# Performance work log

Hardware: AMD Instinct MI355X
Metric: run time of the kernel (lower is better)

Reference implementation:

```python
import jax, jax.numpy as jnp
import numpy as np

USER_NUM = 100000
ITEM_NUM = 50000
N_NODES = USER_NUM + ITEM_NUM
EMB = 64
NNZ = 5_000_000


def setup_inputs() -> dict:
    key = jax.random.key(0)
    k1, k2, k3, k4, k5 = jax.random.split(key, 5)
    user_emb = jax.random.normal(k1, (USER_NUM, EMB), dtype=jnp.float32) * 0.1
    item_emb = jax.random.normal(k2, (ITEM_NUM, EMB), dtype=jnp.float32) * 0.1
    adj_row = jax.random.randint(k3, (NNZ,), 0, N_NODES, dtype=jnp.int32)
    adj_col = jax.random.randint(k4, (NNZ,), 0, N_NODES, dtype=jnp.int32)
    # normalized-adjacency-like positive values
    adj_vals = jax.random.uniform(k5, (NNZ,), dtype=jnp.float32) / 32.0
    return {
        "user_emb": user_emb,
        "item_emb": item_emb,
        "adj_row": adj_row,
        "adj_col": adj_col,
        "adj_vals": adj_vals,
        "n_layers": 3,
    }


def _spmm(row, col, vals, x, n):
    # y = A @ x with A in COO: gather source rows, scale, scatter-add to dest rows
    gathered = x[col] * vals[:, None]  # [nnz, emb]
    return jax.ops.segment_sum(gathered, row, num_segments=n)


def reference(user_emb, item_emb, adj_row, adj_col, adj_vals, n_layers):
    ego = jnp.concatenate([user_emb, item_emb], axis=0)  # [N, emb]
    acc = ego  # running sum over layer outputs (fused stack+mean)
    for _ in range(n_layers):
        ego = _spmm(adj_row, adj_col, adj_vals, ego, N_NODES)
        acc = acc + ego
    all_emb = acc / jnp.asarray(n_layers + 1, dtype=acc.dtype)
    return all_emb[:USER_NUM], all_emb[USER_NUM:]
```

## Files before the change

### kernel.cpp

```cpp
#include <hip/hip_runtime.h>

#define USER_NUM 100000
#define ITEM_NUM 50000
#define N_NODES  150000
#define EMB      64
#define NNZ      5000000
#define NELEM    (N_NODES * EMB)

#define K        1024
#define RPB      147
#define T        8192
#define BST      512
#define NT       ((NNZ + T - 1) / T)
#define SB_CAP   8192

typedef float     vf4 __attribute__((ext_vector_type(4)));
typedef _Float16  vh4 __attribute__((ext_vector_type(4)));
typedef _Float16  half_t;

__global__ void concat_kernel(const float* __restrict__ user,
                              const float* __restrict__ item,
                              float* __restrict__ A, half_t* __restrict__ H0) {
    int i = blockIdx.x * blockDim.x + threadIdx.x;
    if (i >= NELEM / 4) return;
    int base = i * 4;
    const float* src = (base < USER_NUM * EMB) ? (user + base)
                                               : (item + (base - USER_NUM * EMB));
    vf4 v = __builtin_nontemporal_load((const vf4*)src);
    __builtin_nontemporal_store(v, (vf4*)(A + base));
    vh4 h;
    h[0] = (half_t)v[0]; h[1] = (half_t)v[1]; h[2] = (half_t)v[2]; h[3] = (half_t)v[3];
    __builtin_nontemporal_store(h, (vh4*)(H0 + base));
}

__global__ __launch_bounds__(256) void hist_kernel(const int* __restrict__ row,
                                                   int* __restrict__ bucketcnt) {
    __shared__ int h[K];
    for (int i = threadIdx.x; i < K; i += 256) h[i] = 0;
    __syncthreads();
    int stride = gridDim.x * 256;
    for (int e = blockIdx.x * 256 + threadIdx.x; e < NNZ; e += stride) {
        int b = __builtin_nontemporal_load(row + e) / RPB;
        atomicAdd(&h[b], 1);
    }
    __syncthreads();
    for (int i = threadIdx.x; i < K; i += 256)
        if (h[i]) atomicAdd(&bucketcnt[i], h[i]);
}

__global__ __launch_bounds__(256) void scan_buckets(const int* __restrict__ bucketcnt,
                                                    int* __restrict__ gbase,
                                                    int* __restrict__ gcursor) {
    __shared__ int c4[K];
    __shared__ int ps[256];
    int t = threadIdx.x;
    for (int i = t; i < K; i += 256) c4[i] = bucketcnt[i];
    __syncthreads();
    int s = c4[4*t] + c4[4*t+1] + c4[4*t+2] + c4[4*t+3];
    ps[t] = s;
    __syncthreads();
    for (int ofs = 1; ofs < 256; ofs <<= 1) {
        int tv = (t >= ofs) ? ps[t - ofs] : 0;
        __syncthreads();
        ps[t] += tv;
        __syncthreads();
    }
    int run = ps[t] - s;
    for (int k = 0; k < 4; ++k) {
        int b = 4*t + k;
        gbase[b] = run; gcursor[b] = run;
        run += c4[b];
    }
    if (t == 255) gbase[K] = run;
}

__global__ __launch_bounds__(BST) void bin_scatter(const int* __restrict__ row,
                                                   const int* __restrict__ col,
                                                   const float* __restrict__ vals,
                                                   int* __restrict__ gcursor,
                                                   long long* __restrict__ sedge) {
    __shared__ long long      staged[T];
    __shared__ int            srow[T];
    __shared__ unsigned short bs[T];
    __shared__ int cnt[K];
    __shared__ int cbase[K];
    __shared__ int gb[K];
    __shared__ int ps[BST];
    int tid = threadIdx.x;
    int e0 = blockIdx.x * T;
    int e1 = e0 + T; if (e1 > NNZ) e1 = NNZ;
    int n = e1 - e0;

    for (int i = tid; i < K; i += BST) cnt[i] = 0;
    __syncthreads();
    for (int e = e0 + tid; e < e1; e += BST) {
        int r = __builtin_nontemporal_load(row + e);
        srow[e - e0] = r;
        atomicAdd(&cnt[r / RPB], 1);
    }
    __syncthreads();
    int b0 = 2 * tid, b1 = b0 + 1;
    int c0 = cnt[b0], c1 = cnt[b1];
    int s = c0 + c1;
    ps[tid] = s;
    __syncthreads();
    for (int ofs = 1; ofs < BST; ofs <<= 1) {
        int tv = (tid >= ofs) ? ps[tid - ofs] : 0;
        __syncthreads();
        ps[tid] += tv;
        __syncthreads();
    }
    int run = ps[tid] - s;
    cbase[b0] = run;       cbase[b1] = run + c0;
    gb[b0] = c0 ? atomicAdd(&gcursor[b0], c0) : 0;
    gb[b1] = c1 ? atomicAdd(&gcursor[b1], c1) : 0;
    cnt[b0] = run;         cnt[b1] = run + c0;
    __syncthreads();
    for (int i = tid; i < n; i += BST) {
        int   r = srow[i];
        int   c = __builtin_nontemporal_load(col + e0 + i);
        float v = __builtin_nontemporal_load(vals + e0 + i);
        int b  = r / RPB;
        int ro = r - b * RPB;
        int slot = atomicAdd(&cnt[b], 1);
        staged[slot] = (long long)(unsigned)(c | (ro << 18))
                     | ((long long)__float_as_int(v) << 32);
        bs[slot] = (unsigned short)b;
    }
    __syncthreads();
    for (int i = tid; i < n; i += BST) {
        int b = bs[i];
        long long pv = staged[i];
        int dst = gb[b] + (i - cbase[b]);
        __builtin_nontemporal_store(pv, sedge + dst);
    }
}

__global__ __launch_bounds__(256) void sort_bucket(const int* __restrict__ gbase,
                                                   long long* __restrict__ sedge,
                                                   int* __restrict__ rowend,
                                                   long long* __restrict__ gscratch) {
    __shared__ long long staged[SB_CAP];
    __shared__ int rcnt[RPB];
    __shared__ int rbase[RPB + 1];
    __shared__ int rcur[RPB];
    int b = blockIdx.x;
    int s = gbase[b], e = gbase[b + 1];
    int n = e - s;
    int rowbase = b * RPB;
    int nr = N_NODES - rowbase;
    if (nr > RPB) nr = RPB;
    if (nr < 0) nr = 0;
    int tid = threadIdx.x;
    for (int i = tid; i < RPB; i += 256) rcnt[i] = 0;
    __syncthreads();
    for (int i = tid; i < n; i += 256) {
        int ro = (int)((sedge[s + i] >> 18) & 0xFF);
        atomicAdd(&rcnt[ro], 1);
    }
    __syncthreads();
    if (tid == 0) {
        int run = 0;
        for (int i = 0; i < RPB; ++i) { rbase[i] = run; run += rcnt[i]; }
        rbase[RPB] = run;
    }
    __syncthreads();
    for (int i = tid; i < nr; i += 256)
        rowend[rowbase + i] = s + rbase[i + 1];
    for (int i = tid; i < RPB; i += 256) rcur[i] = rbase[i];
    __syncthreads();
    if (n <= SB_CAP) {
        for (int i = tid; i < n; i += 256) {
            long long p = sedge[s + i];
            int ro = (int)((p >> 18) & 0xFF);
            int slot = atomicAdd(&rcur[ro], 1);
            staged[slot] = p & 0xFFFFFFFF0003FFFFLL;
        }
        __syncthreads();
        for (int i = tid; i < n; i += 256)
            __builtin_nontemporal_store(staged[i], sedge + s + i);
    } else {
        for (int i = tid; i < n; i += 256) {
            long long p = sedge[s + i];
            int ro = (int)((p >> 18) & 0xFF);
            int slot = atomicAdd(&rcur[ro], 1);
            gscratch[s + slot] = p & 0xFFFFFFFF0003FFFFLL;
        }
        __syncthreads();
        for (int i = tid; i < n; i += 256)
            sedge[s + i] = gscratch[s + i];
    }
}

template <int MODE>
__global__ __launch_bounds__(256) void spmm_row_kernel(
        const int* __restrict__ rowend,
        const long long* __restrict__ sedge,
        const half_t* __restrict__ xh,
        const float* __restrict__ xf,
        half_t* __restrict__ ynext, float* __restrict__ acc) {
    int wave = threadIdx.x >> 6;
    int lane = threadIdx.x & 63;
    int r = blockIdx.x * 4 + wave;
    if (r >= N_NODES) return;
    int start = (r == 0) ? 0 : rowend[r - 1];
    int end = rowend[r];
    float s = 0.f;
    for (int base = start; base < end; base += 64) {
        int n = end - base; if (n > 64) n = 64;
        int c = 0; float v = 0.f;
        if (lane < n) {
            long long pv = __builtin_nontemporal_load(sedge + base + lane);
            c = (int)(unsigned int)(pv & 0xffffffffLL);
            v = __int_as_float((int)(pv >> 32));
        }
        int j = 0;
        for (; j + 16 <= n; j += 16) {
            int ck[16]; float vk[16];
#pragma unroll
            for (int k = 0; k < 16; ++k) { ck[k] = __shfl(c, j + k); vk[k] = __shfl(v, j + k); }
            float xk[16];
#pragma unroll
            for (int k = 0; k < 16; ++k) xk[k] = (float)xh[ck[k] * EMB + lane];
#pragma unroll
            for (int k = 0; k < 16; ++k) s += vk[k] * xk[k];
        }
        for (; j + 4 <= n; j += 4) {
            int   c0 = __shfl(c, j),     c1 = __shfl(c, j + 1);
            int   c2 = __shfl(c, j + 2), c3 = __shfl(c, j + 3);
            float v0 = __shfl(v, j),     v1 = __shfl(v, j + 1);
            float v2 = __shfl(v, j + 2), v3 = __shfl(v, j + 3);
            float x0 = (float)xh[c0 * EMB + lane];
            float x1 = (float)xh[c1 * EMB + lane];
            float x2 = (float)xh[c2 * EMB + lane];
            float x3 = (float)xh[c3 * EMB + lane];
            s += v0 * x0; s += v1 * x1; s += v2 * x2; s += v3 * x3;
        }
        for (; j < n; ++j) {
            int   cj = __shfl(c, j);
            float vj = __shfl(v, j);
            s += vj * (float)xh[cj * EMB + lane];
        }
    }
    int o = r * EMB + lane;
    if (MODE == 1) {
        ynext[o] = (half_t)s;
        __builtin_nontemporal_store(xf[o] + s, acc + o);
    } else if (MODE == 2) {
        ynext[o] = (half_t)s;
        float a = __builtin_nontemporal_load(acc + o);
        __builtin_nontemporal_store(a + s, acc + o);
    } else {
        float a = __builtin_nontemporal_load(acc + o);
        __builtin_nontemporal_store((a + s) * 0.25f, acc + o);
    }
}

extern "C" void kernel_launch(void* const* d_in, const int* in_sizes, int n_in,
                              void* d_out, int out_size, void* d_ws, size_t ws_size,
                              hipStream_t stream) {
    const float* user = (const float*)d_in[0];
    const float* item = (const float*)d_in[1];
    const int*   row  = (const int*)d_in[2];
    const int*   col  = (const int*)d_in[3];
    const float* vals = (const float*)d_in[4];

    float*     A         = (float*)d_ws;
    half_t*    H0        = (half_t*)(A + NELEM);
    half_t*    H1        = H0 + NELEM;
    long long* sedge     = (long long*)(H1 + NELEM);
    int*       bucketcnt = (int*)(sedge + NNZ);
    int*       gbase     = bucketcnt + K;
    int*       gcursor   = gbase + (K + 1);
    int*       rowend    = gcursor + K;
    float*     acc       = (float*)d_out;

    const int eb = 256;
    const int cgrid = (NELEM / 4 + eb - 1) / eb;
    const int rgrid = N_NODES / 4;

    hipMemsetAsync(bucketcnt, 0, K * sizeof(int), stream);
    hist_kernel<<<640, eb, 0, stream>>>(row, bucketcnt);
    scan_buckets<<<1, eb, 0, stream>>>(bucketcnt, gbase, gcursor);
    bin_scatter<<<NT, BST, 0, stream>>>(row, col, vals, gcursor, sedge);
    sort_bucket<<<K, eb, 0, stream>>>(gbase, sedge, rowend, (long long*)A);
    concat_kernel<<<cgrid, eb, 0, stream>>>(user, item, A, H0);

    spmm_row_kernel<1><<<rgrid, eb, 0, stream>>>(rowend, sedge, H0, A, H1, acc);
    spmm_row_kernel<2><<<rgrid, eb, 0, stream>>>(rowend, sedge, H1, nullptr, H0, acc);
    spmm_row_kernel<3><<<rgrid, eb, 0, stream>>>(rowend, sedge, H0, nullptr, nullptr, acc);
}
```

Before: 648.8 us.

## Use wave-uniform scalar edge loads in SpMM and shrink bin_scatter LDS footprint

The SpMM row kernel makes row bounds wave-uniform with readfirstlane and reads each packed edge directly with uniform (scalar-eligible) loads in groups of 8. This replaces the per-lane vector load plus shuffle broadcast. The column index is masked to 18 bits, which fixes decoding when the bin_scatter packing puts the row offset in the upper bits of the low word. bin_scatter no longer stages row indices in LDS and re-reads them from global memory instead, and the tile size drops from 8192 to 6144 to raise occupancy. The trade is an extra global read of the row array against lower LDS use, and shallower 8-edge prefetch against the previous 16-wide batching.

```diff
diff --git a/kernel.cpp b/kernel.cpp
--- a/kernel.cpp
+++ b/kernel.cpp
@@ -9,7 +9,7 @@
 
 #define K        1024
 #define RPB      147
-#define T        8192
+#define T        6144
 #define BST      512
 #define NT       ((NNZ + T - 1) / T)
 #define SB_CAP   8192
@@ -80,7 +80,6 @@
                                                    int* __restrict__ gcursor,
                                                    long long* __restrict__ sedge) {
     __shared__ long long      staged[T];
-    __shared__ int            srow[T];
     __shared__ unsigned short bs[T];
     __shared__ int cnt[K];
     __shared__ int cbase[K];
@@ -95,7 +94,6 @@
     __syncthreads();
     for (int e = e0 + tid; e < e1; e += BST) {
         int r = __builtin_nontemporal_load(row + e);
-        srow[e - e0] = r;
         atomicAdd(&cnt[r / RPB], 1);
     }
     __syncthreads();
@@ -116,10 +114,10 @@
     gb[b1] = c1 ? atomicAdd(&gcursor[b1], c1) : 0;
     cnt[b0] = run;         cnt[b1] = run + c0;
     __syncthreads();
-    for (int i = tid; i < n; i += BST) {
-        int   r = srow[i];
-        int   c = __builtin_nontemporal_load(col + e0 + i);
-        float v = __builtin_nontemporal_load(vals + e0 + i);
+    for (int e = e0 + tid; e < e1; e += BST) {
+        int   r = __builtin_nontemporal_load(row + e);
+        int   c = __builtin_nontemporal_load(col + e);
+        float v = __builtin_nontemporal_load(vals + e);
         int b  = r / RPB;
         int ro = r - b * RPB;
         int slot = atomicAdd(&cnt[b], 1);
@@ -203,44 +201,27 @@
     int lane = threadIdx.x & 63;
     int r = blockIdx.x * 4 + wave;
     if (r >= N_NODES) return;
-    int start = (r == 0) ? 0 : rowend[r - 1];
-    int end = rowend[r];
+    int start = __builtin_amdgcn_readfirstlane((r == 0) ? 0 : rowend[r - 1]);
+    int end   = __builtin_amdgcn_readfirstlane(rowend[r]);
     float s = 0.f;
-    for (int base = start; base < end; base += 64) {
-        int n = end - base; if (n > 64) n = 64;
-        int c = 0; float v = 0.f;
-        if (lane < n) {
-            long long pv = __builtin_nontemporal_load(sedge + base + lane);
-            c = (int)(unsigned int)(pv & 0xffffffffLL);
-            v = __int_as_float((int)(pv >> 32));
+    int j = start;
+    for (; j + 8 <= end; j += 8) {
+        const long long* ep = sedge + j;
+        long long pk[8];
+#pragma unroll
+        for (int k = 0; k < 8; ++k) pk[k] = ep[k];
+#pragma unroll
+        for (int k = 0; k < 8; ++k) {
+            unsigned cx = (unsigned)pk[k];
+            float vv = __int_as_float((int)(pk[k] >> 32));
+            s += vv * (float)xh[(cx & 0x3FFFFu) * EMB + lane];
         }
-        int j = 0;
-        for (; j + 16 <= n; j += 16) {
-            int ck[16]; float vk[16];
-#pragma unroll
-            for (int k = 0; k < 16; ++k) { ck[k] = __shfl(c, j + k); vk[k] = __shfl(v, j + k); }
-            float xk[16];
-#pragma unroll
-            for (int k = 0; k < 16; ++k) xk[k] = (float)xh[ck[k] * EMB + lane];
-#pragma unroll
-            for (int k = 0; k < 16; ++k) s += vk[k] * xk[k];
-        }
-        for (; j + 4 <= n; j += 4) {
-            int   c0 = __shfl(c, j),     c1 = __shfl(c, j + 1);
-            int   c2 = __shfl(c, j + 2), c3 = __shfl(c, j + 3);
-            float v0 = __shfl(v, j),     v1 = __shfl(v, j + 1);
-            float v2 = __shfl(v, j + 2), v3 = __shfl(v, j + 3);
-            float x0 = (float)xh[c0 * EMB + lane];
-            float x1 = (float)xh[c1 * EMB + lane];
-            float x2 = (float)xh[c2 * EMB + lane];
-            float x3 = (float)xh[c3 * EMB + lane];
-            s += v0 * x0; s += v1 * x1; s += v2 * x2; s += v3 * x3;
-        }
-        for (; j < n; ++j) {
-            int   cj = __shfl(c, j);
-            float vj = __shfl(v, j);
-            s += vj * (float)xh[cj * EMB + lane];
-        }
+    }
+    for (; j < end; ++j) {
+        long long p = sedge[j];
+        unsigned cx = (unsigned)p;
+        float vv = __int_as_float((int)(p >> 32));
+        s += vv * (float)xh[(cx & 0x3FFFFu) * EMB + lane];
     }
     int o = r * EMB + lane;
     if (MODE == 1) {
```

Result: no change. 645.6 us (-0.5%).
